# Kernel optimization log

Hardware: AMD Instinct MI355X
Metric: run time of the kernel (lower is better)

## Reference

```python
import jax, jax.numpy as jnp
import numpy as np

HID, KQ, V = 1024, 64, 64
B, S = 8, 2048
NEG_INF = -1000000000.0


def setup_inputs() -> dict:
    key = jax.random.key(0)
    ks = jax.random.split(key, 10)
    return {
        "k_hidden_inputs": jax.random.normal(ks[0], (B, S, HID), jnp.float32),
        "q_hidden_inputs": jax.random.normal(ks[1], (B, S, HID), jnp.float32),
        "v_hidden_inputs": jax.random.normal(ks[2], (B, S, HID), jnp.float32),
        "mask": jax.random.randint(ks[3], (B, S, S), 0, 2, jnp.int32),
        "Wq": jax.random.normal(ks[4], (HID, KQ), jnp.float32) * 0.02,
        "bq": jnp.zeros((KQ,), jnp.float32),
        "Wk": jax.random.normal(ks[5], (HID, KQ), jnp.float32) * 0.02,
        "bk": jnp.zeros((KQ,), jnp.float32),
        "Wv": jax.random.normal(ks[6], (HID, V), jnp.float32) * 0.02,
        "bv": jnp.zeros((V,), jnp.float32),
    }


def reference(k_hidden_inputs, q_hidden_inputs, v_hidden_inputs, mask,
              Wq, bq, Wk, bk, Wv, bv):
    keys = jnp.einsum('bsh,hd->bsd', k_hidden_inputs, Wk) + bk
    queries = jnp.einsum('bsh,hd->bsd', q_hidden_inputs, Wq) + bq
    values = jnp.einsum('bsh,hd->bsd', v_hidden_inputs, Wv) + bv
    # scaled dot-product scores: [B, S_q, S_k]
    scores = jnp.einsum('bqd,bkd->bqk', queries, keys) / jnp.sqrt(jnp.float32(KQ))
    scores = jnp.where(mask == 0, jnp.float32(NEG_INF), scores)
    attn = jax.nn.softmax(scores, axis=-1)
    return jnp.einsum('bqk,bkv->bqv', attn, values)
```

## Files before the change

kernel.cpp:

```cpp
#include <hip/hip_runtime.h>

#define HIDDEN 1024
#define NB 8
#define SEQ 2048
#define DH 64

typedef long long i64;
typedef unsigned short u16;
typedef __attribute__((ext_vector_type(8))) _Float16 half8;
typedef __attribute__((ext_vector_type(4))) float f32x4;

#define MFMA16F __builtin_amdgcn_mfma_f32_16x16x32_f16

__device__ __forceinline__ u16 f2h(float x) {
    _Float16 h = (_Float16)x;
    return __builtin_bit_cast(u16, h);
}
__device__ __forceinline__ void gl_lds16(const void* g, void* l) {
    __builtin_amdgcn_global_load_lds(
        (const __attribute__((address_space(1))) unsigned int*)g,
        (__attribute__((address_space(3))) unsigned int*)l, 16, 0, 0);
}

__global__ __launch_bounds__(256) void wimg_prep16(
    const float* __restrict__ Wq, const float* __restrict__ Wk, const float* __restrict__ Wv,
    u16* __restrict__ Wimg)
{
    const int t = blockIdx.x * 256 + threadIdx.x;
    const int te = t >> 13;
    const int rem = t & 8191;
    const int p = rem >> 9;
    const int rem2 = rem & 511;
    const int n = rem2 >> 3;
    const int pos = rem2 & 7;
    const float* W = te == 0 ? Wq : te == 1 ? Wk : Wv;
    const int g = pos ^ (n & 7);
    const int k0 = p * 64 + g * 8;
    u16* dst = Wimg + (i64)t * 8;
    #pragma unroll
    for (int j = 0; j < 8; ++j)
        dst[j] = f2h(W[(i64)(k0 + j) * DH + n]);
}

__global__ __launch_bounds__(64) void proj_mfma10(
    const float* __restrict__ qh, const float* __restrict__ kh, const float* __restrict__ vh,
    const u16* __restrict__ Wimg,
    const float* __restrict__ bq, const float* __restrict__ bk, const float* __restrict__ bv,
    u16* __restrict__ Qb, u16* __restrict__ Kb, u16* __restrict__ Vt)
{
    const int te = blockIdx.y;
    const float* A    = te == 0 ? qh : te == 1 ? kh : vh;
    const float* bias = te == 0 ? bq : te == 1 ? bk : bv;
    const int row0 = blockIdx.x << 4;
    const int lane = threadIdx.x;
    const int lr = lane & 15, lg = lane >> 4;

    __shared__ __attribute__((aligned(16))) float AL[2][1024];
    __shared__ __attribute__((aligned(16))) u16  WL[2][4096];

    const u16* Wte = Wimg + (i64)te * 16 * 4096;

    const float* asrc[4];
    #pragma unroll
    for (int i = 0; i < 4; ++i) {
        const int ar = 4 * i + (lane >> 4);
        const int ab = (lane & 15) ^ (ar & 15);
        asrc[i] = A + (i64)(row0 + ar) * HIDDEN + (ab << 2);
    }
    const u16* wsrc = Wte + (lane << 3);

    f32x4 acc[4] = {};

#define STAGE(S, B) { \
        _Pragma("unroll") \
        for (int i_ = 0; i_ < 4; ++i_) \
            gl_lds16(asrc[i_] + (S) * 64, &AL[B][i_ * 256]); \
        _Pragma("unroll") \
        for (int j_ = 0; j_ < 8; ++j_) \
            gl_lds16(wsrc + (S) * 4096 + j_ * 512, &WL[B][j_ * 512]); }

    STAGE(0, 0)

    #pragma unroll 1
    for (int s = 0; s < 16; ++s) {
        const int buf = s & 1;
        if (s < 15) {
            STAGE(s + 1, buf ^ 1)
            asm volatile("s_waitcnt vmcnt(12)" ::: "memory");
        } else {
            asm volatile("s_waitcnt vmcnt(0)" ::: "memory");
        }
        #pragma unroll
        for (int ks = 0; ks < 2; ++ks) {
            const int b0 = ks * 8 + lg * 2;
            const float4 fa = *(const float4*)&AL[buf][lr * 64 + ((b0 ^ lr) << 2)];
            const float4 fb = *(const float4*)&AL[buf][lr * 64 + (((b0 + 1) ^ lr) << 2)];
            half8 a;
            a[0] = (_Float16)fa.x; a[1] = (_Float16)fa.y;
            a[2] = (_Float16)fa.z; a[3] = (_Float16)fa.w;
            a[4] = (_Float16)fb.x; a[5] = (_Float16)fb.y;
            a[6] = (_Float16)fb.z; a[7] = (_Float16)fb.w;
            #pragma unroll
            for (int nt = 0; nt < 4; ++nt) {
                const int n = nt * 16 + lr;
                const int pos = (ks * 4 + lg) ^ (n & 7);
                const half8 b = *(const half8*)&WL[buf][n * 64 + (pos << 3)];
                acc[nt] = MFMA16F(a, b, acc[nt], 0, 0, 0);
            }
        }
    }
#undef STAGE

    #pragma unroll
    for (int nt = 0; nt < 4; ++nt) {
        const int col = nt * 16 + lr;
        const float bb = bias[col];
        #pragma unroll
        for (int r = 0; r < 4; ++r) {
            const i64 grow = row0 + (lg << 2) + r;
            const u16 v = f2h(acc[nt][r] + bb);
            if (te == 0)      Qb[grow * DH + col] = v;
            else if (te == 1) Kb[grow * DH + col] = v;
            else {
                const i64 bb2 = grow >> 11, key = grow & 2047;
                Vt[(bb2 * DH + col) * SEQ + key] = v;
            }
        }
    }
}

__global__ __launch_bounds__(64) void attn_mfma(
    const u16* __restrict__ Qb, const u16* __restrict__ Kb, const u16* __restrict__ Vt,
    const int* __restrict__ mask, float* __restrict__ out)
{
    __shared__ __attribute__((aligned(16))) u16 Kl[2][64 * 64];
    __shared__ __attribute__((aligned(16))) u16 Vl[2][64 * 64];
    __shared__ __attribute__((aligned(16))) u16 Pl[16][72];

    const int lane = threadIdx.x;
    const int lr = lane & 15, lg = lane >> 4;
    const int b  = blockIdx.x >> 7;
    const int q0 = (blockIdx.x & 127) << 4;

    const i64 qrow = (i64)b * SEQ + q0 + lr;
    const half8 qf0 = *(const half8*)(Qb + qrow * DH + lg * 8);
    const half8 qf1 = *(const half8*)(Qb + qrow * DH + 32 + lg * 8);

    const int srow = lane >> 3;
    const int scb  = lane & 7;

    f32x4 oacc[4] = {};
    float rs0 = 0.f, rs1 = 0.f, rs2 = 0.f, rs3 = 0.f;

    {
        const i64 kbase = (i64)b * SEQ;
        #pragma unroll
        for (int i = 0; i < 8; ++i) {
            int row = i * 8 + srow, cb = scb ^ (row & 7);
            gl_lds16(Kb + (kbase + row) * DH + cb * 8, &Kl[0][i * 512]);
        }
        #pragma unroll
        for (int i = 0; i < 8; ++i) {
            int row = i * 8 + srow, cb = scb ^ (row & 7);
            gl_lds16(Vt + ((i64)b * DH + row) * SEQ + cb * 8, &Vl[0][i * 512]);
        }
    }

    #pragma unroll 1
    for (int t = 0; t < 32; ++t) {
        const int kt = t * 64;
        const int buf = t & 1;

        int mv[16];
        #pragma unroll
        for (int tt = 0; tt < 4; ++tt)
            #pragma unroll
            for (int r = 0; r < 4; ++r)
                mv[tt * 4 + r] =
                    mask[((i64)b * SEQ + q0 + lg * 4 + r) * SEQ + kt + tt * 16 + lr];

        if (t < 31) {
            const int kn = kt + 64;
            const i64 kbase = (i64)b * SEQ + kn;
            #pragma unroll
            for (int i = 0; i < 8; ++i) {
                int row = i * 8 + srow, cb = scb ^ (row & 7);
                gl_lds16(Kb + (kbase + row) * DH + cb * 8, &Kl[buf ^ 1][i * 512]);
            }
            #pragma unroll
            for (int i = 0; i < 8; ++i) {
                int row = i * 8 + srow, cb = scb ^ (row & 7);
                gl_lds16(Vt + ((i64)b * DH + row) * SEQ + kn + cb * 8, &Vl[buf ^ 1][i * 512]);
            }
            asm volatile("s_waitcnt vmcnt(32)" ::: "memory");
        } else {
            asm volatile("s_waitcnt vmcnt(16)" ::: "memory");
        }

        f32x4 sacc[4] = {};
        #pragma unroll
        for (int tt = 0; tt < 4; ++tt) {
            int row = tt * 16 + lr, x = row & 7;
            half8 k0 = *(const half8*)&Kl[buf][row * 64 + ((lg) ^ x) * 8];
            half8 k1 = *(const half8*)&Kl[buf][row * 64 + ((lg + 4) ^ x) * 8];
            sacc[tt] = MFMA16F(qf0, k0, sacc[tt], 0, 0, 0);
            sacc[tt] = MFMA16F(qf1, k1, sacc[tt], 0, 0, 0);
        }

        #pragma unroll
        for (int tt = 0; tt < 4; ++tt) {
            #pragma unroll
            for (int r = 0; r < 4; ++r) {
                float p = (mv[tt * 4 + r] != 0) ? __expf(sacc[tt][r] * 0.125f) : 0.0f;
                if      (r == 0) rs0 += p;
                else if (r == 1) rs1 += p;
                else if (r == 2) rs2 += p;
                else             rs3 += p;
                Pl[lg * 4 + r][tt * 16 + lr] = f2h(p);
            }
        }

        const half8 p0 = *(const half8*)&Pl[lr][lg * 8];
        const half8 p1 = *(const half8*)&Pl[lr][32 + lg * 8];
        #pragma unroll
        for (int vt = 0; vt < 4; ++vt) {
            int row = vt * 16 + lr, x = row & 7;
            half8 v0 = *(const half8*)&Vl[buf][row * 64 + ((lg) ^ x) * 8];
            half8 v1 = *(const half8*)&Vl[buf][row * 64 + ((lg + 4) ^ x) * 8];
            oacc[vt] = MFMA16F(p0, v0, oacc[vt], 0, 0, 0);
            oacc[vt] = MFMA16F(p1, v1, oacc[vt], 0, 0, 0);
        }
    }

    float rs[4] = {rs0, rs1, rs2, rs3};
    #pragma unroll
    for (int r = 0; r < 4; ++r) {
        float v = rs[r];
        v += __shfl_xor(v, 1, 64);
        v += __shfl_xor(v, 2, 64);
        v += __shfl_xor(v, 4, 64);
        v += __shfl_xor(v, 8, 64);
        rs[r] = 1.0f / v;
    }
    #pragma unroll
    for (int vt = 0; vt < 4; ++vt)
        #pragma unroll
        for (int r = 0; r < 4; ++r)
            out[((i64)b * SEQ + q0 + lg * 4 + r) * DH + vt * 16 + lr] = oacc[vt][r] * rs[r];
}

extern "C" void kernel_launch(void* const* d_in, const int* in_sizes, int n_in,
                              void* d_out, int out_size, void* d_ws, size_t ws_size,
                              hipStream_t stream) {
    const float* kh   = (const float*)d_in[0];
    const float* qh   = (const float*)d_in[1];
    const float* vh   = (const float*)d_in[2];
    const int*   mask = (const int*)  d_in[3];
    const float* Wq   = (const float*)d_in[4];
    const float* bq   = (const float*)d_in[5];
    const float* Wk   = (const float*)d_in[6];
    const float* bk   = (const float*)d_in[7];
    const float* Wv   = (const float*)d_in[8];
    const float* bv   = (const float*)d_in[9];
    float* out = (float*)d_out;

    u16* Wimg = (u16*)d_ws;
    u16* Qb   = Wimg + 3 * 16 * 4096;
    u16* Kb   = Qb + (i64)NB * SEQ * DH;
    u16* Vt   = Kb + (i64)NB * SEQ * DH;

    wimg_prep16<<<96, 256, 0, stream>>>(Wq, Wk, Wv, Wimg);
    proj_mfma10<<<dim3(1024, 3), 64, 0, stream>>>(qh, kh, vh, Wimg,
                                                  bq, bk, bv, Qb, Kb, Vt);
    attn_mfma<<<1024, 64, 0, stream>>>(Qb, Kb, Vt, mask, out);
}
```

Before: 122.5 us.

## Deepen activation prefetch in projection kernel to five LDS stages

Splits the projection kernel's staging so activation tiles use a five-deep LDS ring buffer while the weight tiles stay double-buffered. A prologue, a steady-state loop with adjusted vmcnt waits, and an explicit drain epilogue replace the simple two-stage loop. The goal is to keep more global loads in flight and hide HBM latency on the bandwidth-bound fp32 activation reads. The cost is more LDS per block, which may lower the number of resident blocks per CU.

```diff
diff --git a/kernel.cpp b/kernel.cpp
--- a/kernel.cpp
+++ b/kernel.cpp
@@ -42,7 +42,7 @@
         dst[j] = f2h(W[(i64)(k0 + j) * DH + n]);
 }
 
-__global__ __launch_bounds__(64) void proj_mfma10(
+__global__ __launch_bounds__(64) void proj_mfma11(
     const float* __restrict__ qh, const float* __restrict__ kh, const float* __restrict__ vh,
     const u16* __restrict__ Wimg,
     const float* __restrict__ bq, const float* __restrict__ bk, const float* __restrict__ bv,
@@ -55,7 +55,7 @@
     const int lane = threadIdx.x;
     const int lr = lane & 15, lg = lane >> 4;
 
-    __shared__ __attribute__((aligned(16))) float AL[2][1024];
+    __shared__ __attribute__((aligned(16))) float AL[5][1024];
     __shared__ __attribute__((aligned(16))) u16  WL[2][4096];
 
     const u16* Wte = Wimg + (i64)te * 16 * 4096;
@@ -71,45 +71,69 @@
 
     f32x4 acc[4] = {};
 
-#define STAGE(S, B) { \
+#define STAGE_A(S, B) { \
         _Pragma("unroll") \
         for (int i_ = 0; i_ < 4; ++i_) \
-            gl_lds16(asrc[i_] + (S) * 64, &AL[B][i_ * 256]); \
+            gl_lds16(asrc[i_] + (S) * 64, &AL[B][i_ * 256]); }
+#define STAGE_W(S, B) { \
         _Pragma("unroll") \
         for (int j_ = 0; j_ < 8; ++j_) \
             gl_lds16(wsrc + (S) * 4096 + j_ * 512, &WL[B][j_ * 512]); }
 
-    STAGE(0, 0)
-
+#define COMPUTE(AB, WB) { \
+        _Pragma("unroll") \
+        for (int ks = 0; ks < 2; ++ks) { \
+            const int b0 = ks * 8 + lg * 2; \
+            const float4 fa = *(const float4*)&AL[AB][lr * 64 + ((b0 ^ lr) << 2)]; \
+            const float4 fb = *(const float4*)&AL[AB][lr * 64 + (((b0 + 1) ^ lr) << 2)]; \
+            half8 a; \
+            a[0] = (_Float16)fa.x; a[1] = (_Float16)fa.y; \
+            a[2] = (_Float16)fa.z; a[3] = (_Float16)fa.w; \
+            a[4] = (_Float16)fb.x; a[5] = (_Float16)fb.y; \
+            a[6] = (_Float16)fb.z; a[7] = (_Float16)fb.w; \
+            _Pragma("unroll") \
+            for (int nt = 0; nt < 4; ++nt) { \
+                const int n = nt * 16 + lr; \
+                const int pos = (ks * 4 + lg) ^ (n & 7); \
+                const half8 b = *(const half8*)&WL[WB][n * 64 + (pos << 3)]; \
+                acc[nt] = MFMA16F(a, b, acc[nt], 0, 0, 0); \
+            } \
+        } }
+
+    STAGE_A(0, 0) STAGE_A(1, 1) STAGE_A(2, 2) STAGE_A(3, 3)
+    STAGE_W(0, 0)
+
+    STAGE_W(1, 1)
+    STAGE_A(4, 4)
+    asm volatile("s_waitcnt vmcnt(12)" ::: "memory");
+    COMPUTE(0, 0)
+
+    int ab_use = 1, ab_stage = 0;
     #pragma unroll 1
-    for (int s = 0; s < 16; ++s) {
-        const int buf = s & 1;
-        if (s < 15) {
-            STAGE(s + 1, buf ^ 1)
-            asm volatile("s_waitcnt vmcnt(12)" ::: "memory");
-        } else {
-            asm volatile("s_waitcnt vmcnt(0)" ::: "memory");
-        }
-        #pragma unroll
-        for (int ks = 0; ks < 2; ++ks) {
-            const int b0 = ks * 8 + lg * 2;
-            const float4 fa = *(const float4*)&AL[buf][lr * 64 + ((b0 ^ lr) << 2)];
-            const float4 fb = *(const float4*)&AL[buf][lr * 64 + (((b0 + 1) ^ lr) << 2)];
-            half8 a;
-            a[0] = (_Float16)fa.x; a[1] = (_Float16)fa.y;
-            a[2] = (_Float16)fa.z; a[3] = (_Float16)fa.w;
-            a[4] = (_Float16)fb.x; a[5] = (_Float16)fb.y;
-            a[6] = (_Float16)fb.z; a[7] = (_Float16)fb.w;
-            #pragma unroll
-            for (int nt = 0; nt < 4; ++nt) {
-                const int n = nt * 16 + lr;
-                const int pos = (ks * 4 + lg) ^ (n & 7);
-                const half8 b = *(const half8*)&WL[buf][n * 64 + (pos << 3)];
-                acc[nt] = MFMA16F(a, b, acc[nt], 0, 0, 0);
-            }
-        }
-    }
-#undef STAGE
+    for (int s = 1; s < 12; ++s) {
+        STAGE_W(s + 1, (s + 1) & 1)
+        STAGE_A(s + 4, ab_stage)
+        asm volatile("s_waitcnt vmcnt(16)" ::: "memory");
+        COMPUTE(ab_use, s & 1)
+        if (++ab_use == 5) ab_use = 0;
+        if (++ab_stage == 5) ab_stage = 0;
+    }
+
+    STAGE_W(13, 1)
+    asm volatile("s_waitcnt vmcnt(12)" ::: "memory");
+    COMPUTE(2, 0)
+    STAGE_W(14, 0)
+    asm volatile("s_waitcnt vmcnt(8)" ::: "memory");
+    COMPUTE(3, 1)
+    STAGE_W(15, 1)
+    asm volatile("s_waitcnt vmcnt(8)" ::: "memory");
+    COMPUTE(4, 0)
+    asm volatile("s_waitcnt vmcnt(0)" ::: "memory");
+    COMPUTE(0, 1)
+
+#undef STAGE_A
+#undef STAGE_W
+#undef COMPUTE
 
     #pragma unroll
     for (int nt = 0; nt < 4; ++nt) {
@@ -270,7 +294,7 @@
     u16* Vt   = Kb + (i64)NB * SEQ * DH;
 
     wimg_prep16<<<96, 256, 0, stream>>>(Wq, Wk, Wv, Wimg);
-    proj_mfma10<<<dim3(1024, 3), 64, 0, stream>>>(qh, kh, vh, Wimg,
+    proj_mfma11<<<dim3(1024, 3), 64, 0, stream>>>(qh, kh, vh, Wimg,
                                                   bq, bk, bv, Qb, Kb, Vt);
     attn_mfma<<<1024, 64, 0, stream>>>(Qb, Kb, Vt, mask, out);
 }
```

Result: slower. 126.5 us (+3.3%).
